# Performance work log

Hardware: AMD Instinct MI355X
Metric: run time of the kernel (lower is better)

## Reference

```python
import jax, jax.numpy as jnp
import numpy as np


def _conv(x, w, b, padding='SAME' if False else 'VALID'):
    # NCHW conv, OIHW weights
    out = jax.lax.conv_general_dilated(
        x, w, window_strides=(1, 1), padding=padding,
        dimension_numbers=('NCHW', 'OIHW', 'NCHW'))
    return out + b[None, :, None, None]


def setup_inputs() -> dict:
    key = jax.random.key(0)
    ks = jax.random.split(key, 14)
    s = lambda k, shape, scale=0.1: jax.random.normal(k, shape, dtype=jnp.float32) * scale
    return {
        'x': jax.random.normal(ks[0], (8, 16, 512, 512), dtype=jnp.float32),
        'y': jax.random.normal(ks[1], (8, 5, 512, 512), dtype=jnp.float32),
        'fuse_w': s(ks[2], (16, 5, 1, 1)),
        'fuse_b': s(ks[3], (16,)),
        'se_w1': s(ks[4], (16, 16)),
        'se_w2': s(ks[5], (5, 16)),
        'bd_w': s(ks[6], (2, 5, 1, 1)),
        'bd_b': s(ks[7], (2,)),
        'fc_w': s(ks[8], (16, 32, 3, 3)),
        'fc_b': s(ks[9], (16,)),
        'fm_w': s(ks[10], (2, 16, 1, 1)),
        'fm_b': s(ks[11], (2,)),
        'cv_w': s(ks[12], (16, 1, 1, 1)),
        'cv_b': s(ks[13], (16,)),
    }


def reference(x, y, fuse_w, fuse_b, se_w1, se_w2, bd_w, bd_b,
              fc_w, fc_b, fm_w, fm_b, cv_w, cv_b):
    # fuse: 1x1 conv 5->16 + ReLU
    fuse_box = jax.nn.relu(_conv(y, fuse_w, fuse_b, 'VALID'))  # [B,16,H,W]
    # global average pool -> SE mimic MLP -> sigmoid gate over 5 channels
    gap = jnp.mean(fuse_box, axis=(2, 3))                       # [B,16]
    se = jax.nn.sigmoid(jax.nn.relu(gap @ se_w1.T) @ se_w2.T)   # [B,5]
    feat_se = y * se[:, :, None, None]                          # [B,5,H,W]
    # boundary head: 1x1 conv 5->2, softmax over channel, take fg prob
    boundary = _conv(feat_se, bd_w, bd_b, 'VALID')              # [B,2,H,W]
    boundary_scale = jax.nn.softmax(boundary, axis=1)[:, 1:2]   # [B,1,H,W]
    # mask head: concat(x, fuse_box) -> 3x3 conv 32->16 + ReLU -> 1x1 conv 16->2
    feat_concat = jnp.concatenate([x, fuse_box], axis=1)        # [B,32,H,W]
    fcc = jax.nn.relu(_conv(feat_concat, fc_w, fc_b, 'SAME'))   # [B,16,H,W]
    mask = _conv(fcc, fm_w, fm_b, 'VALID')                      # [B,2,H,W]
    mask_scale = jax.nn.softmax(mask, axis=1)[:, 1:2]           # [B,1,H,W]
    # fused scale factor, clamp, expand to 16 channels via 1x1 conv
    scalefactor = jnp.clip(mask_scale + boundary_scale, 0.0, 1.0)
    return _conv(scalefactor, cv_w, cv_b, 'VALID')              # [B,16,H,W]
```

## Files before the change

### kernel.cpp

```cpp
#include <hip/hip_runtime.h>
#include <hip/hip_bf16.h>

#define HW 262144
#define IW 512
#define TW 64
#define TH 8
#define HLW 66
#define NHALO 660
#define ROWU 40

typedef __attribute__((ext_vector_type(8))) short short8;
typedef __attribute__((ext_vector_type(4))) float f32x4;
typedef __attribute__((ext_vector_type(4))) unsigned int uint4v;

static __device__ inline unsigned int bpack2(float a, float b) {
  __hip_bfloat16 ha = __float2bfloat16(a);
  __hip_bfloat16 hb = __float2bfloat16(b);
  unsigned short ua = *reinterpret_cast<unsigned short*>(&ha);
  unsigned short ub = *reinterpret_cast<unsigned short*>(&hb);
  return (unsigned int)ua | ((unsigned int)ub << 16);
}

__global__ __launch_bounds__(256) void k_gap(
    const float* __restrict__ y, const float* __restrict__ fuse_w,
    const float* __restrict__ fuse_b, float* __restrict__ partial) {
  __shared__ float fw[80], fb[16];
  __shared__ float red[4][16];
  int tid = threadIdx.x;
  if (tid < 80) fw[tid] = fuse_w[tid];
  if (tid < 16) fb[tid] = fuse_b[tid];
  __syncthreads();

  int b = blockIdx.x >> 7;
  int chunk = blockIdx.x & 127;
  const float* yb = y + (size_t)b * 5 * HW + chunk * 2048;

  float sums[16];
#pragma unroll
  for (int o = 0; o < 16; ++o) sums[o] = 0.f;

  for (int i = 0; i < 2048; i += 256) {
    int p = i + tid;
    float yv[5];
#pragma unroll
    for (int c = 0; c < 5; ++c) yv[c] = yb[c * HW + p];
#pragma unroll
    for (int o = 0; o < 16; ++o) {
      float a = fb[o];
#pragma unroll
      for (int c = 0; c < 5; ++c) a = fmaf(fw[o * 5 + c], yv[c], a);
      sums[o] += fmaxf(a, 0.f);
    }
  }

  int lane = tid & 63, wv = tid >> 6;
#pragma unroll
  for (int o = 0; o < 16; ++o) {
    float v = sums[o];
    for (int off = 32; off > 0; off >>= 1) v += __shfl_down(v, off);
    if (lane == 0) red[wv][o] = v;
  }
  __syncthreads();
  if (tid < 16)
    partial[blockIdx.x * 16 + tid] =
        red[0][tid] + red[1][tid] + red[2][tid] + red[3][tid];
}

__global__ __launch_bounds__(256) void k_se(
    const float* __restrict__ partial, const float* __restrict__ se_w1,
    const float* __restrict__ se_w2, const float* __restrict__ bd_w,
    float* __restrict__ bd_eff) {
  int tid = threadIdx.x;
  int b = tid >> 5, sub = tid & 31;
  float g[16];
#pragma unroll
  for (int c = 0; c < 16; ++c) g[c] = 0.f;
#pragma unroll
  for (int k = 0; k < 4; ++k) {
    const float* p = partial + (b * 128 + sub + k * 32) * 16;
#pragma unroll
    for (int c = 0; c < 16; ++c) g[c] += p[c];
  }
#pragma unroll
  for (int c = 0; c < 16; ++c) {
    float v = g[c];
    v += __shfl_xor(v, 1);  v += __shfl_xor(v, 2);
    v += __shfl_xor(v, 4);  v += __shfl_xor(v, 8);
    v += __shfl_xor(v, 16);
    g[c] = v * (1.f / 262144.f);
  }
  if (sub == 0) {
    float h[16];
#pragma unroll
    for (int j = 0; j < 16; ++j) {
      float s = 0.f;
#pragma unroll
      for (int c = 0; c < 16; ++c) s += g[c] * se_w1[j * 16 + c];
      h[j] = fmaxf(s, 0.f);
    }
#pragma unroll
    for (int i = 0; i < 5; ++i) {
      float s = 0.f;
#pragma unroll
      for (int j = 0; j < 16; ++j) s += h[j] * se_w2[i * 16 + j];
      float se = 1.f / (1.f + expf(-s));
      bd_eff[b * 10 + i]     = bd_w[i] * se;
      bd_eff[b * 10 + 5 + i] = bd_w[5 + i] * se;
    }
  }
}

__global__ void k_prep(const float* __restrict__ fc_w,
                       unsigned short* __restrict__ wTab) {
  int i = blockIdx.x * 256 + threadIdx.x;
  if (i < 4608) {
    int ci = i & 31, rest = i >> 5;
    int oc = rest & 15, s = rest >> 4;
    float v = fc_w[(oc * 32 + ci) * 9 + s];
    __hip_bfloat16 h = __float2bfloat16(v);
    wTab[i] = *reinterpret_cast<unsigned short*>(&h);
  }
}

__global__ __launch_bounds__(256) void k_pre(
    const float* __restrict__ y, const float* __restrict__ fuse_w,
    const float* __restrict__ fuse_b, const float* __restrict__ bd_eff,
    const float* __restrict__ bd_b, unsigned short* __restrict__ fuseP,
    float* __restrict__ bscaleP) {
  __shared__ float fw[80], fb[16], bde[10], bdb[2];
  int tid = threadIdx.x;
  int b = blockIdx.x >> 7;
  if (tid < 80) fw[tid] = fuse_w[tid];
  else if (tid < 96)  fb[tid - 80]  = fuse_b[tid - 80];
  else if (tid < 106) bde[tid - 96] = bd_eff[b * 10 + tid - 96];
  else if (tid < 108) bdb[tid - 106] = bd_b[tid - 106];
  __syncthreads();

  const float* yb = y + (size_t)b * 5 * HW;
  int gof0 = (blockIdx.x & 127) * 2048;
#pragma unroll 1
  for (int i = 0; i < 2048; i += 256) {
    int gofs = gof0 + i + tid;
    float yv[5];
#pragma unroll
    for (int c = 0; c < 5; ++c) yv[c] = yb[c * HW + gofs];
    float fo[16];
#pragma unroll
    for (int o = 0; o < 16; ++o) {
      float a = fb[o];
#pragma unroll
      for (int c = 0; c < 5; ++c) a = fmaf(fw[o * 5 + c], yv[c], a);
      fo[o] = fmaxf(a, 0.f);
    }
    size_t po = ((size_t)b * HW + gofs) * 16;
    uint4v v0 = {bpack2(fo[0], fo[1]), bpack2(fo[2], fo[3]),
                 bpack2(fo[4], fo[5]), bpack2(fo[6], fo[7])};
    uint4v v1 = {bpack2(fo[8], fo[9]), bpack2(fo[10], fo[11]),
                 bpack2(fo[12], fo[13]), bpack2(fo[14], fo[15])};
    *reinterpret_cast<uint4v*>(fuseP + po) = v0;
    *reinterpret_cast<uint4v*>(fuseP + po + 8) = v1;
    float bl0 = bdb[0], bl1 = bdb[1];
#pragma unroll
    for (int c = 0; c < 5; ++c) {
      bl0 = fmaf(bde[c], yv[c], bl0);
      bl1 = fmaf(bde[5 + c], yv[c], bl1);
    }
    bscaleP[(size_t)b * HW + gofs] = 1.f / (1.f + __expf(bl0 - bl1));
  }
}

template <int PRE>
__global__ __launch_bounds__(256) void k_main(
    const float* __restrict__ x, const float* __restrict__ y,
    const float* __restrict__ fuse_w, const float* __restrict__ fuse_b,
    const unsigned short* __restrict__ wTab,
    const unsigned short* __restrict__ fuseP,
    const float* __restrict__ bscaleP,
    const float* __restrict__ bd_eff, const float* __restrict__ bd_b,
    const float* __restrict__ fc_b,
    const float* __restrict__ fm_w, const float* __restrict__ fm_b,
    const float* __restrict__ cv_w, const float* __restrict__ cv_b,
    float* __restrict__ out) {
  __shared__ unsigned short tile[NHALO * ROWU];
  __shared__ float s_fw[80], s_fb[16], s_bde[10], s_bdb[2], s_fm[32],
      s_fmb[2], s_cv[16], s_cvb[16], s_fcb[16];

  int tid = threadIdx.x;
  int bsel = blockIdx.z;
  int h0 = blockIdx.y * TH;
  int w0 = blockIdx.x * TW;

  if (tid < 80) s_fw[tid] = fuse_w[tid];
  else if (tid < 96)  s_fb[tid - 80]   = fuse_b[tid - 80];
  else if (tid < 106) s_bde[tid - 96]  = bd_eff[bsel * 10 + tid - 96];
  else if (tid < 108) s_bdb[tid - 106] = bd_b[tid - 106];
  else if (tid < 140) s_fm[tid - 108]  = fm_w[tid - 108];
  else if (tid < 142) s_fmb[tid - 140] = fm_b[tid - 140];
  else if (tid < 158) s_cv[tid - 142]  = cv_w[tid - 142];
  else if (tid < 174) s_cvb[tid - 158] = cv_b[tid - 158];
  else if (tid < 190) s_fcb[tid - 174] = fc_b[tid - 174];

  int lane = tid & 63, wv = tid >> 6;
  int l15 = lane & 15, q = lane >> 4;

  short8 afrag[9];
#pragma unroll
  for (int s = 0; s < 9; ++s)
    afrag[s] = *reinterpret_cast<const short8*>(wTab + (s * 16 + l15) * 32 + q * 8);

  __syncthreads();

  const float* yb = y + (size_t)bsel * 5 * HW;
  const float* xb = x + (size_t)bsel * 16 * HW;
#pragma unroll 1
  for (int p = tid; p < NHALO; p += 256) {
    int hr = p / HLW, wc = p - hr * HLW;
    int gh = h0 - 1 + hr, gw = w0 - 1 + wc;
    bool valid = (gh >= 0) & (gh < IW) & (gw >= 0) & (gw < IW);
    uint4v* dst = reinterpret_cast<uint4v*>(&tile[p * ROWU]);
    if (valid) {
      int gofs = gh * IW + gw;
      if (PRE) {
        size_t po = ((size_t)bsel * HW + gofs) * 16;
        uint4v f0 = *reinterpret_cast<const uint4v*>(fuseP + po);
        uint4v f1 = *reinterpret_cast<const uint4v*>(fuseP + po + 8);
        float bsc = bscaleP[(size_t)bsel * HW + gofs];
        float a0 = xb[gofs],          a1 = xb[HW + gofs];
        float a2 = xb[2 * HW + gofs], a3 = xb[3 * HW + gofs];
        float a4 = xb[4 * HW + gofs], a5 = xb[5 * HW + gofs];
        float a6 = xb[6 * HW + gofs], a7 = xb[7 * HW + gofs];
        float a8 = xb[8 * HW + gofs],  a9 = xb[9 * HW + gofs];
        float aA = xb[10 * HW + gofs], aB = xb[11 * HW + gofs];
        float aC = xb[12 * HW + gofs], aD = xb[13 * HW + gofs];
        float aE = xb[14 * HW + gofs], aF = xb[15 * HW + gofs];
        dst[0] = uint4v{bpack2(a0, a1), bpack2(a2, a3),
                        bpack2(a4, a5), bpack2(a6, a7)};
        dst[1] = uint4v{bpack2(a8, a9), bpack2(aA, aB),
                        bpack2(aC, aD), bpack2(aE, aF)};
        dst[2] = f0;
        dst[3] = f1;
        *reinterpret_cast<float*>(&tile[p * ROWU + 32]) = bsc;
      } else {
        {
          float a0 = xb[gofs],          a1 = xb[HW + gofs];
          float a2 = xb[2 * HW + gofs], a3 = xb[3 * HW + gofs];
          float a4 = xb[4 * HW + gofs], a5 = xb[5 * HW + gofs];
          float a6 = xb[6 * HW + gofs], a7 = xb[7 * HW + gofs];
          dst[0] = uint4v{bpack2(a0, a1), bpack2(a2, a3),
                          bpack2(a4, a5), bpack2(a6, a7)};
        }
        {
          float a0 = xb[8 * HW + gofs],  a1 = xb[9 * HW + gofs];
          float a2 = xb[10 * HW + gofs], a3 = xb[11 * HW + gofs];
          float a4 = xb[12 * HW + gofs], a5 = xb[13 * HW + gofs];
          float a6 = xb[14 * HW + gofs], a7 = xb[15 * HW + gofs];
          dst[1] = uint4v{bpack2(a0, a1), bpack2(a2, a3),
                          bpack2(a4, a5), bpack2(a6, a7)};
        }
        float yv[5];
#pragma unroll
        for (int c = 0; c < 5; ++c) yv[c] = yb[c * HW + gofs];
        float fo[8];
#pragma unroll
        for (int o = 0; o < 8; ++o) {
          float a = s_fb[o];
#pragma unroll
          for (int c = 0; c < 5; ++c) a = fmaf(s_fw[o * 5 + c], yv[c], a);
          fo[o] = fmaxf(a, 0.f);
        }
        dst[2] = uint4v{bpack2(fo[0], fo[1]), bpack2(fo[2], fo[3]),
                        bpack2(fo[4], fo[5]), bpack2(fo[6], fo[7])};
#pragma unroll
        for (int o = 0; o < 8; ++o) {
          float a = s_fb[8 + o];
#pragma unroll
          for (int c = 0; c < 5; ++c) a = fmaf(s_fw[(8 + o) * 5 + c], yv[c], a);
          fo[o] = fmaxf(a, 0.f);
        }
        dst[3] = uint4v{bpack2(fo[0], fo[1]), bpack2(fo[2], fo[3]),
                        bpack2(fo[4], fo[5]), bpack2(fo[6], fo[7])};
        float bl0 = s_bdb[0], bl1 = s_bdb[1];
#pragma unroll
        for (int c = 0; c < 5; ++c) {
          bl0 = fmaf(s_bde[c], yv[c], bl0);
          bl1 = fmaf(s_bde[5 + c], yv[c], bl1);
        }
        *reinterpret_cast<float*>(&tile[p * ROWU + 32]) =
            1.f / (1.f + __expf(bl0 - bl1));
      }
    } else {
      uint4v z = {0, 0, 0, 0};
      dst[0] = z; dst[1] = z; dst[2] = z; dst[3] = z;
      *reinterpret_cast<float*>(&tile[p * ROWU + 32]) = 0.f;
    }
  }
  __syncthreads();

  const char* tb = reinterpret_cast<const char*>(tile);
  unsigned bofs[8];
  f32x4 acc[8];
#pragma unroll
  for (int g = 0; g < 8; ++g) {
    int row = 2 * wv + (g >> 2), c0 = (g & 3) * 16;
    bofs[g] = (unsigned)((row * HLW + c0 + l15) * (ROWU * 2) + q * 16);
    acc[g] = f32x4{0.f, 0.f, 0.f, 0.f};
  }
#pragma unroll
  for (int kh = 0; kh < 3; ++kh) {
#pragma unroll
    for (int kw = 0; kw < 3; ++kw) {
      short8 a = afrag[kh * 3 + kw];
#pragma unroll
      for (int g = 0; g < 8; ++g) {
        short8 bfr = *reinterpret_cast<const short8*>(
            tb + bofs[g] + (kh * HLW + kw) * (ROWU * 2));
        acc[g] = __builtin_amdgcn_mfma_f32_16x16x32_bf16(a, bfr, acc[g], 0, 0, 0);
      }
    }
  }

  float pm0[8], pm1[8];
#pragma unroll
  for (int g = 0; g < 8; ++g) {
    float p0 = 0.f, p1 = 0.f;
#pragma unroll
    for (int j = 0; j < 4; ++j) {
      int oc = q * 4 + j;
      float fv = fmaxf(acc[g][j] + s_fcb[oc], 0.f);
      p0 = fmaf(s_fm[oc], fv, p0);
      p1 = fmaf(s_fm[16 + oc], fv, p1);
    }
    pm0[g] = p0; pm1[g] = p1;
  }
#pragma unroll
  for (int g = 0; g < 8; ++g) pm0[g] += __shfl_xor(pm0[g], 16);
#pragma unroll
  for (int g = 0; g < 8; ++g) pm1[g] += __shfl_xor(pm1[g], 16);
#pragma unroll
  for (int g = 0; g < 8; ++g) pm0[g] += __shfl_xor(pm0[g], 32);
#pragma unroll
  for (int g = 0; g < 8; ++g) pm1[g] += __shfl_xor(pm1[g], 32);

  float sc[8];
#pragma unroll
  for (int g = 0; g < 8; ++g) {
    int row = 2 * wv + (g >> 2), c0 = (g & 3) * 16;
    float mscale =
        1.f / (1.f + __expf((pm0[g] + s_fmb[0]) - (pm1[g] + s_fmb[1])));
    float bsc = *reinterpret_cast<const float*>(
        tb + ((row + 1) * HLW + c0 + l15 + 1) * (ROWU * 2) + 64);
    sc[g] = fminf(fmaxf(mscale + bsc, 0.f), 1.f);
  }

  float* outb = out + (size_t)bsel * 16 * HW;
#pragma unroll
  for (int g = 0; g < 8; ++g) {
    int row = 2 * wv + (g >> 2), c0 = (g & 3) * 16;
    int gofs = (h0 + row) * IW + w0 + c0 + l15;
#pragma unroll
    for (int j = 0; j < 4; ++j) {
      int oc = q * 4 + j;
      outb[(size_t)oc * HW + gofs] = fmaf(s_cv[oc], sc[g], s_cvb[oc]);
    }
  }
}

extern "C" void kernel_launch(void* const* d_in, const int* in_sizes, int n_in,
                              void* d_out, int out_size, void* d_ws, size_t ws_size,
                              hipStream_t stream) {
  const float* x      = (const float*)d_in[0];
  const float* y      = (const float*)d_in[1];
  const float* fuse_w = (const float*)d_in[2];
  const float* fuse_b = (const float*)d_in[3];
  const float* se_w1  = (const float*)d_in[4];
  const float* se_w2  = (const float*)d_in[5];
  const float* bd_w   = (const float*)d_in[6];
  const float* bd_b   = (const float*)d_in[7];
  const float* fc_w   = (const float*)d_in[8];
  const float* fc_b   = (const float*)d_in[9];
  const float* fm_w   = (const float*)d_in[10];
  const float* fm_b   = (const float*)d_in[11];
  const float* cv_w   = (const float*)d_in[12];
  const float* cv_b   = (const float*)d_in[13];
  float* out = (float*)d_out;

  char* ws = (char*)d_ws;
  float* partial = (float*)ws;
  float* bd_eff  = partial + 1024 * 16;
  unsigned short* wTab = (unsigned short*)(ws + (1024 * 16 + 80) * 4);
  size_t fuse_off = (((1024 * 16 + 80) * 4 + 4608 * 2) + 255) & ~(size_t)255;
  unsigned short* fuseP = (unsigned short*)(ws + fuse_off);
  float* bscaleP = (float*)(ws + fuse_off + (size_t)2097152 * 32);
  size_t need = fuse_off + (size_t)2097152 * 32 + (size_t)2097152 * 4;
  bool pre = ws_size >= need;

  k_gap<<<1024, 256, 0, stream>>>(y, fuse_w, fuse_b, partial);
  k_se<<<1, 256, 0, stream>>>(partial, se_w1, se_w2, bd_w, bd_eff);
  k_prep<<<18, 256, 0, stream>>>(fc_w, wTab);
  if (pre) {
    k_pre<<<1024, 256, 0, stream>>>(y, fuse_w, fuse_b, bd_eff, bd_b, fuseP,
                                    bscaleP);
    k_main<1><<<dim3(8, 64, 8), 256, 0, stream>>>(
        x, y, fuse_w, fuse_b, wTab, fuseP, bscaleP, bd_eff, bd_b, fc_b, fm_w,
        fm_b, cv_w, cv_b, out);
  } else {
    k_main<0><<<dim3(8, 64, 8), 256, 0, stream>>>(
        x, y, fuse_w, fuse_b, wTab, fuseP, bscaleP, bd_eff, bd_b, fc_b, fm_w,
        fm_b, cv_w, cv_b, out);
  }
}
```

Measured before the change: 144.8 us.

## Pre-pack x and fuse outputs into zero-padded bf16 planes, drop LDS staging

Adds kernels that convert x into two zero-padded bf16 channel-8 planes and write the fuse activations into two more padded planes during the GAP pass. The main conv kernel then reads MFMA B fragments straight from global memory with no shared-memory halo tile or boundary checks. The boundary scale moves into its own kernel. The goal is to remove LDS staging, halo recomputation and the separate fuse recomputation pass. The cost is extra global traffic for the padded planes, several more launches, and reliance on cache hits for the 3x3 overlapping reads.

```diff
diff --git a/kernel.cpp b/kernel.cpp
--- a/kernel.cpp
+++ b/kernel.cpp
@@ -5,9 +5,8 @@
 #define IW 512
 #define TW 64
 #define TH 8
-#define HLW 66
-#define NHALO 660
-#define ROWU 40
+#define PW 514
+#define PP 264196
 
 typedef __attribute__((ext_vector_type(8))) short short8;
 typedef __attribute__((ext_vector_type(4))) float f32x4;
@@ -21,9 +20,48 @@
   return (unsigned int)ua | ((unsigned int)ub << 16);
 }
 
-__global__ __launch_bounds__(256) void k_gap(
+__global__ __launch_bounds__(256) void k_zero(uint4v* __restrict__ xP0,
+                                              uint4v* __restrict__ xP1,
+                                              uint4v* __restrict__ fP0,
+                                              uint4v* __restrict__ fP1) {
+  int pl = blockIdx.x >> 3, b = blockIdx.x & 7;
+  uint4v* base = (pl == 0 ? xP0 : pl == 1 ? xP1 : pl == 2 ? fP0 : fP1) +
+                 (size_t)b * PP;
+  uint4v z = {0, 0, 0, 0};
+  for (int i = threadIdx.x; i < 2052; i += 256) {
+    int pp;
+    if (i < 514) pp = i;
+    else if (i < 1028) pp = 513 * PW + (i - 514);
+    else if (i < 1540) pp = (i - 1028 + 1) * PW;
+    else pp = (i - 1540 + 1) * PW + 513;
+    base[pp] = z;
+  }
+}
+
+__global__ __launch_bounds__(256) void k_xc(const float* __restrict__ x,
+                                            uint4v* __restrict__ xP0,
+                                            uint4v* __restrict__ xP1) {
+  for (int it = 0; it < 4; ++it) {
+    int idx = blockIdx.x * 1024 + it * 256 + threadIdx.x;
+    int b = idx >> 18, gofs = idx & (HW - 1);
+    const float* xb = x + (size_t)b * 16 * HW + gofs;
+    int gh = gofs >> 9, gw = gofs & 511;
+    size_t pp = (size_t)b * PP + (gh + 1) * PW + gw + 1;
+    float a0 = xb[0],       a1 = xb[HW],      a2 = xb[2 * HW],  a3 = xb[3 * HW];
+    float a4 = xb[4 * HW],  a5 = xb[5 * HW],  a6 = xb[6 * HW],  a7 = xb[7 * HW];
+    xP0[pp] = uint4v{bpack2(a0, a1), bpack2(a2, a3), bpack2(a4, a5),
+                     bpack2(a6, a7)};
+    float b0 = xb[8 * HW],  b1 = xb[9 * HW],  b2 = xb[10 * HW], b3 = xb[11 * HW];
+    float b4 = xb[12 * HW], b5 = xb[13 * HW], b6 = xb[14 * HW], b7 = xb[15 * HW];
+    xP1[pp] = uint4v{bpack2(b0, b1), bpack2(b2, b3), bpack2(b4, b5),
+                     bpack2(b6, b7)};
+  }
+}
+
+__global__ __launch_bounds__(256) void k_fuse(
     const float* __restrict__ y, const float* __restrict__ fuse_w,
-    const float* __restrict__ fuse_b, float* __restrict__ partial) {
+    const float* __restrict__ fuse_b, uint4v* __restrict__ fP0,
+    uint4v* __restrict__ fP1, float* __restrict__ partial) {
   __shared__ float fw[80], fb[16];
   __shared__ float red[4][16];
   int tid = threadIdx.x;
@@ -31,26 +69,37 @@
   if (tid < 16) fb[tid] = fuse_b[tid];
   __syncthreads();
 
-  int b = blockIdx.x >> 7;
-  int chunk = blockIdx.x & 127;
-  const float* yb = y + (size_t)b * 5 * HW + chunk * 2048;
+  int b = blockIdx.x >> 7, chunk = blockIdx.x & 127;
+  const float* yb = y + (size_t)b * 5 * HW;
+  uint4v* f0 = fP0 + (size_t)b * PP;
+  uint4v* f1 = fP1 + (size_t)b * PP;
+  int gof0 = chunk * 2048;
 
   float sums[16];
 #pragma unroll
   for (int o = 0; o < 16; ++o) sums[o] = 0.f;
 
+#pragma unroll 1
   for (int i = 0; i < 2048; i += 256) {
-    int p = i + tid;
+    int gofs = gof0 + i + tid;
     float yv[5];
 #pragma unroll
-    for (int c = 0; c < 5; ++c) yv[c] = yb[c * HW + p];
+    for (int c = 0; c < 5; ++c) yv[c] = yb[c * HW + gofs];
+    float fo[16];
 #pragma unroll
     for (int o = 0; o < 16; ++o) {
       float a = fb[o];
 #pragma unroll
       for (int c = 0; c < 5; ++c) a = fmaf(fw[o * 5 + c], yv[c], a);
-      sums[o] += fmaxf(a, 0.f);
-    }
+      fo[o] = fmaxf(a, 0.f);
+      sums[o] += fo[o];
+    }
+    int gh = gofs >> 9, gw = gofs & 511;
+    int pp = (gh + 1) * PW + gw + 1;
+    f0[pp] = uint4v{bpack2(fo[0], fo[1]), bpack2(fo[2], fo[3]),
+                    bpack2(fo[4], fo[5]), bpack2(fo[6], fo[7])};
+    f1[pp] = uint4v{bpack2(fo[8], fo[9]), bpack2(fo[10], fo[11]),
+                    bpack2(fo[12], fo[13]), bpack2(fo[14], fo[15])};
   }
 
   int lane = tid & 63, wv = tid >> 6;
@@ -107,6 +156,32 @@
       bd_eff[b * 10 + i]     = bd_w[i] * se;
       bd_eff[b * 10 + 5 + i] = bd_w[5 + i] * se;
     }
+  }
+}
+
+__global__ __launch_bounds__(256) void k_bsc(const float* __restrict__ y,
+                                             const float* __restrict__ bd_eff,
+                                             const float* __restrict__ bd_b,
+                                             float* __restrict__ bscaleP) {
+  __shared__ float bde[10], bdb[2];
+  int tid = threadIdx.x;
+  int b = blockIdx.x >> 7, chunk = blockIdx.x & 127;
+  if (tid < 10) bde[tid] = bd_eff[b * 10 + tid];
+  if (tid < 2) bdb[tid] = bd_b[tid];
+  __syncthreads();
+  const float* yb = y + (size_t)b * 5 * HW;
+  int gof0 = chunk * 2048;
+#pragma unroll 1
+  for (int i = 0; i < 2048; i += 256) {
+    int gofs = gof0 + i + tid;
+    float bl0 = bdb[0], bl1 = bdb[1];
+#pragma unroll
+    for (int c = 0; c < 5; ++c) {
+      float yv = yb[c * HW + gofs];
+      bl0 = fmaf(bde[c], yv, bl0);
+      bl1 = fmaf(bde[5 + c], yv, bl1);
+    }
+    bscaleP[(size_t)b * HW + gofs] = 1.f / (1.f + __expf(bl0 - bl1));
   }
 }
 
@@ -122,60 +197,146 @@
   }
 }
 
-__global__ __launch_bounds__(256) void k_pre(
+__global__ __launch_bounds__(256) void k_main2(
+    const unsigned short* __restrict__ xP0, const unsigned short* __restrict__ xP1,
+    const unsigned short* __restrict__ fP0, const unsigned short* __restrict__ fP1,
+    const unsigned short* __restrict__ wTab, const float* __restrict__ bscaleP,
+    const float* __restrict__ fc_b, const float* __restrict__ fm_w,
+    const float* __restrict__ fm_b, const float* __restrict__ cv_w,
+    const float* __restrict__ cv_b, float* __restrict__ out) {
+  __shared__ float s_fm[32], s_fmb[2], s_cv[16], s_cvb[16], s_fcb[16];
+  int tid = threadIdx.x;
+  if (tid < 32) s_fm[tid] = fm_w[tid];
+  else if (tid < 34) s_fmb[tid - 32] = fm_b[tid - 32];
+  else if (tid < 50) s_cv[tid - 34]  = cv_w[tid - 34];
+  else if (tid < 66) s_cvb[tid - 50] = cv_b[tid - 50];
+  else if (tid < 82) s_fcb[tid - 66] = fc_b[tid - 66];
+
+  int bsel = blockIdx.z;
+  int h0 = blockIdx.y * TH;
+  int w0 = blockIdx.x * TW;
+  int lane = tid & 63, wv = tid >> 6;
+  int l15 = lane & 15, q = lane >> 4;
+
+  short8 afrag[9];
+#pragma unroll
+  for (int s = 0; s < 9; ++s)
+    afrag[s] = *reinterpret_cast<const short8*>(wTab + (s * 16 + l15) * 32 + q * 8);
+
+  const unsigned short* plane = q == 0 ? xP0 : q == 1 ? xP1 : q == 2 ? fP0 : fP1;
+  const short8* pl = reinterpret_cast<const short8*>(plane) + (size_t)bsel * PP;
+
+  __syncthreads();
+
+  int pb[8];
+  f32x4 acc[8];
+#pragma unroll
+  for (int g = 0; g < 8; ++g) {
+    int row = 2 * wv + (g >> 2), c0 = (g & 3) * 16;
+    pb[g] = (h0 + row) * PW + w0 + c0 + l15;
+    acc[g] = f32x4{0.f, 0.f, 0.f, 0.f};
+  }
+#pragma unroll
+  for (int kh = 0; kh < 3; ++kh) {
+#pragma unroll
+    for (int kw = 0; kw < 3; ++kw) {
+      short8 a = afrag[kh * 3 + kw];
+      short8 bf[8];
+#pragma unroll
+      for (int g = 0; g < 8; ++g) bf[g] = pl[pb[g] + kh * PW + kw];
+#pragma unroll
+      for (int g = 0; g < 8; ++g)
+        acc[g] = __builtin_amdgcn_mfma_f32_16x16x32_bf16(a, bf[g], acc[g], 0, 0, 0);
+    }
+  }
+
+  float pm0[8], pm1[8];
+#pragma unroll
+  for (int g = 0; g < 8; ++g) {
+    float p0 = 0.f, p1 = 0.f;
+#pragma unroll
+    for (int j = 0; j < 4; ++j) {
+      int oc = q * 4 + j;
+      float fv = fmaxf(acc[g][j] + s_fcb[oc], 0.f);
+      p0 = fmaf(s_fm[oc], fv, p0);
+      p1 = fmaf(s_fm[16 + oc], fv, p1);
+    }
+    pm0[g] = p0; pm1[g] = p1;
+  }
+#pragma unroll
+  for (int g = 0; g < 8; ++g) pm0[g] += __shfl_xor(pm0[g], 16);
+#pragma unroll
+  for (int g = 0; g < 8; ++g) pm1[g] += __shfl_xor(pm1[g], 16);
+#pragma unroll
+  for (int g = 0; g < 8; ++g) pm0[g] += __shfl_xor(pm0[g], 32);
+#pragma unroll
+  for (int g = 0; g < 8; ++g) pm1[g] += __shfl_xor(pm1[g], 32);
+
+  const float* bsb = bscaleP + (size_t)bsel * HW;
+  float* outb = out + (size_t)bsel * 16 * HW;
+#pragma unroll
+  for (int g = 0; g < 8; ++g) {
+    int row = 2 * wv + (g >> 2), c0 = (g & 3) * 16;
+    int gofs = (h0 + row) * IW + w0 + c0 + l15;
+    float mscale =
+        1.f / (1.f + __expf((pm0[g] + s_fmb[0]) - (pm1[g] + s_fmb[1])));
+    float sc = fminf(fmaxf(mscale + bsb[gofs], 0.f), 1.f);
+#pragma unroll
+    for (int j = 0; j < 4; ++j) {
+      int oc = q * 4 + j;
+      outb[(size_t)oc * HW + gofs] = fmaf(s_cv[oc], sc, s_cvb[oc]);
+    }
+  }
+}
+
+#define HLW 66
+#define NHALO 660
+#define ROWU 40
+
+__global__ __launch_bounds__(256) void k_gap(
     const float* __restrict__ y, const float* __restrict__ fuse_w,
-    const float* __restrict__ fuse_b, const float* __restrict__ bd_eff,
-    const float* __restrict__ bd_b, unsigned short* __restrict__ fuseP,
-    float* __restrict__ bscaleP) {
-  __shared__ float fw[80], fb[16], bde[10], bdb[2];
+    const float* __restrict__ fuse_b, float* __restrict__ partial) {
+  __shared__ float fw[80], fb[16];
+  __shared__ float red[4][16];
   int tid = threadIdx.x;
-  int b = blockIdx.x >> 7;
   if (tid < 80) fw[tid] = fuse_w[tid];
-  else if (tid < 96)  fb[tid - 80]  = fuse_b[tid - 80];
-  else if (tid < 106) bde[tid - 96] = bd_eff[b * 10 + tid - 96];
-  else if (tid < 108) bdb[tid - 106] = bd_b[tid - 106];
-  __syncthreads();
-
-  const float* yb = y + (size_t)b * 5 * HW;
-  int gof0 = (blockIdx.x & 127) * 2048;
-#pragma unroll 1
+  if (tid < 16) fb[tid] = fuse_b[tid];
+  __syncthreads();
+  int b = blockIdx.x >> 7, chunk = blockIdx.x & 127;
+  const float* yb = y + (size_t)b * 5 * HW + chunk * 2048;
+  float sums[16];
+#pragma unroll
+  for (int o = 0; o < 16; ++o) sums[o] = 0.f;
   for (int i = 0; i < 2048; i += 256) {
-    int gofs = gof0 + i + tid;
+    int p = i + tid;
     float yv[5];
 #pragma unroll
-    for (int c = 0; c < 5; ++c) yv[c] = yb[c * HW + gofs];
-    float fo[16];
+    for (int c = 0; c < 5; ++c) yv[c] = yb[c * HW + p];
 #pragma unroll
     for (int o = 0; o < 16; ++o) {
       float a = fb[o];
 #pragma unroll
       for (int c = 0; c < 5; ++c) a = fmaf(fw[o * 5 + c], yv[c], a);
-      fo[o] = fmaxf(a, 0.f);
-    }
-    size_t po = ((size_t)b * HW + gofs) * 16;
-    uint4v v0 = {bpack2(fo[0], fo[1]), bpack2(fo[2], fo[3]),
-                 bpack2(fo[4], fo[5]), bpack2(fo[6], fo[7])};
-    uint4v v1 = {bpack2(fo[8], fo[9]), bpack2(fo[10], fo[11]),
-                 bpack2(fo[12], fo[13]), bpack2(fo[14], fo[15])};
-    *reinterpret_cast<uint4v*>(fuseP + po) = v0;
-    *reinterpret_cast<uint4v*>(fuseP + po + 8) = v1;
-    float bl0 = bdb[0], bl1 = bdb[1];
-#pragma unroll
-    for (int c = 0; c < 5; ++c) {
-      bl0 = fmaf(bde[c], yv[c], bl0);
-      bl1 = fmaf(bde[5 + c], yv[c], bl1);
-    }
-    bscaleP[(size_t)b * HW + gofs] = 1.f / (1.f + __expf(bl0 - bl1));
-  }
-}
-
-template <int PRE>
-__global__ __launch_bounds__(256) void k_main(
+      sums[o] += fmaxf(a, 0.f);
+    }
+  }
+  int lane = tid & 63, wv = tid >> 6;
+#pragma unroll
+  for (int o = 0; o < 16; ++o) {
+    float v = sums[o];
+    for (int off = 32; off > 0; off >>= 1) v += __shfl_down(v, off);
+    if (lane == 0) red[wv][o] = v;
+  }
+  __syncthreads();
+  if (tid < 16)
+    partial[blockIdx.x * 16 + tid] =
+        red[0][tid] + red[1][tid] + red[2][tid] + red[3][tid];
+}
+
+__global__ __launch_bounds__(256) void k_main_fb(
     const float* __restrict__ x, const float* __restrict__ y,
     const float* __restrict__ fuse_w, const float* __restrict__ fuse_b,
     const unsigned short* __restrict__ wTab,
-    const unsigned short* __restrict__ fuseP,
-    const float* __restrict__ bscaleP,
     const float* __restrict__ bd_eff, const float* __restrict__ bd_b,
     const float* __restrict__ fc_b,
     const float* __restrict__ fm_w, const float* __restrict__ fm_b,
@@ -184,12 +345,8 @@
   __shared__ unsigned short tile[NHALO * ROWU];
   __shared__ float s_fw[80], s_fb[16], s_bde[10], s_bdb[2], s_fm[32],
       s_fmb[2], s_cv[16], s_cvb[16], s_fcb[16];
-
   int tid = threadIdx.x;
-  int bsel = blockIdx.z;
-  int h0 = blockIdx.y * TH;
-  int w0 = blockIdx.x * TW;
-
+  int bsel = blockIdx.z, h0 = blockIdx.y * TH, w0 = blockIdx.x * TW;
   if (tid < 80) s_fw[tid] = fuse_w[tid];
   else if (tid < 96)  s_fb[tid - 80]   = fuse_b[tid - 80];
   else if (tid < 106) s_bde[tid - 96]  = bd_eff[bsel * 10 + tid - 96];
@@ -199,17 +356,12 @@
   else if (tid < 158) s_cv[tid - 142]  = cv_w[tid - 142];
   else if (tid < 174) s_cvb[tid - 158] = cv_b[tid - 158];
   else if (tid < 190) s_fcb[tid - 174] = fc_b[tid - 174];
-
-  int lane = tid & 63, wv = tid >> 6;
-  int l15 = lane & 15, q = lane >> 4;
-
+  int lane = tid & 63, wv = tid >> 6, l15 = lane & 15, q = lane >> 4;
   short8 afrag[9];
 #pragma unroll
   for (int s = 0; s < 9; ++s)
     afrag[s] = *reinterpret_cast<const short8*>(wTab + (s * 16 + l15) * 32 + q * 8);
-
-  __syncthreads();
-
+  __syncthreads();
   const float* yb = y + (size_t)bsel * 5 * HW;
   const float* xb = x + (size_t)bsel * 16 * HW;
 #pragma unroll 1
@@ -220,74 +372,52 @@
     uint4v* dst = reinterpret_cast<uint4v*>(&tile[p * ROWU]);
     if (valid) {
       int gofs = gh * IW + gw;
-      if (PRE) {
-        size_t po = ((size_t)bsel * HW + gofs) * 16;
-        uint4v f0 = *reinterpret_cast<const uint4v*>(fuseP + po);
-        uint4v f1 = *reinterpret_cast<const uint4v*>(fuseP + po + 8);
-        float bsc = bscaleP[(size_t)bsel * HW + gofs];
+      {
         float a0 = xb[gofs],          a1 = xb[HW + gofs];
         float a2 = xb[2 * HW + gofs], a3 = xb[3 * HW + gofs];
         float a4 = xb[4 * HW + gofs], a5 = xb[5 * HW + gofs];
         float a6 = xb[6 * HW + gofs], a7 = xb[7 * HW + gofs];
-        float a8 = xb[8 * HW + gofs],  a9 = xb[9 * HW + gofs];
-        float aA = xb[10 * HW + gofs], aB = xb[11 * HW + gofs];
-        float aC = xb[12 * HW + gofs], aD = xb[13 * HW + gofs];
-        float aE = xb[14 * HW + gofs], aF = xb[15 * HW + gofs];
         dst[0] = uint4v{bpack2(a0, a1), bpack2(a2, a3),
                         bpack2(a4, a5), bpack2(a6, a7)};
-        dst[1] = uint4v{bpack2(a8, a9), bpack2(aA, aB),
-                        bpack2(aC, aD), bpack2(aE, aF)};
-        dst[2] = f0;
-        dst[3] = f1;
-        *reinterpret_cast<float*>(&tile[p * ROWU + 32]) = bsc;
-      } else {
-        {
-          float a0 = xb[gofs],          a1 = xb[HW + gofs];
-          float a2 = xb[2 * HW + gofs], a3 = xb[3 * HW + gofs];
-          float a4 = xb[4 * HW + gofs], a5 = xb[5 * HW + gofs];
-          float a6 = xb[6 * HW + gofs], a7 = xb[7 * HW + gofs];
-          dst[0] = uint4v{bpack2(a0, a1), bpack2(a2, a3),
-                          bpack2(a4, a5), bpack2(a6, a7)};
-        }
-        {
-          float a0 = xb[8 * HW + gofs],  a1 = xb[9 * HW + gofs];
-          float a2 = xb[10 * HW + gofs], a3 = xb[11 * HW + gofs];
-          float a4 = xb[12 * HW + gofs], a5 = xb[13 * HW + gofs];
-          float a6 = xb[14 * HW + gofs], a7 = xb[15 * HW + gofs];
-          dst[1] = uint4v{bpack2(a0, a1), bpack2(a2, a3),
-                          bpack2(a4, a5), bpack2(a6, a7)};
-        }
-        float yv[5];
-#pragma unroll
-        for (int c = 0; c < 5; ++c) yv[c] = yb[c * HW + gofs];
-        float fo[8];
-#pragma unroll
-        for (int o = 0; o < 8; ++o) {
-          float a = s_fb[o];
-#pragma unroll
-          for (int c = 0; c < 5; ++c) a = fmaf(s_fw[o * 5 + c], yv[c], a);
-          fo[o] = fmaxf(a, 0.f);
-        }
-        dst[2] = uint4v{bpack2(fo[0], fo[1]), bpack2(fo[2], fo[3]),
-                        bpack2(fo[4], fo[5]), bpack2(fo[6], fo[7])};
-#pragma unroll
-        for (int o = 0; o < 8; ++o) {
-          float a = s_fb[8 + o];
-#pragma unroll
-          for (int c = 0; c < 5; ++c) a = fmaf(s_fw[(8 + o) * 5 + c], yv[c], a);
-          fo[o] = fmaxf(a, 0.f);
-        }
-        dst[3] = uint4v{bpack2(fo[0], fo[1]), bpack2(fo[2], fo[3]),
-                        bpack2(fo[4], fo[5]), bpack2(fo[6], fo[7])};
-        float bl0 = s_bdb[0], bl1 = s_bdb[1];
-#pragma unroll
-        for (int c = 0; c < 5; ++c) {
-          bl0 = fmaf(s_bde[c], yv[c], bl0);
-          bl1 = fmaf(s_bde[5 + c], yv[c], bl1);
-        }
-        *reinterpret_cast<float*>(&tile[p * ROWU + 32]) =
-            1.f / (1.f + __expf(bl0 - bl1));
       }
+      {
+        float a0 = xb[8 * HW + gofs],  a1 = xb[9 * HW + gofs];
+        float a2 = xb[10 * HW + gofs], a3 = xb[11 * HW + gofs];
+        float a4 = xb[12 * HW + gofs], a5 = xb[13 * HW + gofs];
+        float a6 = xb[14 * HW + gofs], a7 = xb[15 * HW + gofs];
+        dst[1] = uint4v{bpack2(a0, a1), bpack2(a2, a3),
+                        bpack2(a4, a5), bpack2(a6, a7)};
+      }
+      float yv[5];
+#pragma unroll
+      for (int c = 0; c < 5; ++c) yv[c] = yb[c * HW + gofs];
+      float fo[8];
+#pragma unroll
+      for (int o = 0; o < 8; ++o) {
+        float a = s_fb[o];
+#pragma unroll
+        for (int c = 0; c < 5; ++c) a = fmaf(s_fw[o * 5 + c], yv[c], a);
+        fo[o] = fmaxf(a, 0.f);
+      }
+      dst[2] = uint4v{bpack2(fo[0], fo[1]), bpack2(fo[2], fo[3]),
+                      bpack2(fo[4], fo[5]), bpack2(fo[6], fo[7])};
+#pragma unroll
+      for (int o = 0; o < 8; ++o) {
+        float a = s_fb[8 + o];
+#pragma unroll
+        for (int c = 0; c < 5; ++c) a = fmaf(s_fw[(8 + o) * 5 + c], yv[c], a);
+        fo[o] = fmaxf(a, 0.f);
+      }
+      dst[3] = uint4v{bpack2(fo[0], fo[1]), bpack2(fo[2], fo[3]),
+                      bpack2(fo[4], fo[5]), bpack2(fo[6], fo[7])};
+      float bl0 = s_bdb[0], bl1 = s_bdb[1];
+#pragma unroll
+      for (int c = 0; c < 5; ++c) {
+        bl0 = fmaf(s_bde[c], yv[c], bl0);
+        bl1 = fmaf(s_bde[5 + c], yv[c], bl1);
+      }
+      *reinterpret_cast<float*>(&tile[p * ROWU + 32]) =
+          1.f / (1.f + __expf(bl0 - bl1));
     } else {
       uint4v z = {0, 0, 0, 0};
       dst[0] = z; dst[1] = z; dst[2] = z; dst[3] = z;
@@ -295,7 +425,6 @@
     }
   }
   __syncthreads();
-
   const char* tb = reinterpret_cast<const char*>(tile);
   unsigned bofs[8];
   f32x4 acc[8];
@@ -318,7 +447,6 @@
       }
     }
   }
-
   float pm0[8], pm1[8];
 #pragma unroll
   for (int g = 0; g < 8; ++g) {
@@ -340,27 +468,20 @@
   for (int g = 0; g < 8; ++g) pm0[g] += __shfl_xor(pm0[g], 32);
 #pragma unroll
   for (int g = 0; g < 8; ++g) pm1[g] += __shfl_xor(pm1[g], 32);
-
-  float sc[8];
+  float* outb = out + (size_t)bsel * 16 * HW;
 #pragma unroll
   for (int g = 0; g < 8; ++g) {
     int row = 2 * wv + (g >> 2), c0 = (g & 3) * 16;
+    int gofs = (h0 + row) * IW + w0 + c0 + l15;
     float mscale =
         1.f / (1.f + __expf((pm0[g] + s_fmb[0]) - (pm1[g] + s_fmb[1])));
     float bsc = *reinterpret_cast<const float*>(
         tb + ((row + 1) * HLW + c0 + l15 + 1) * (ROWU * 2) + 64);
-    sc[g] = fminf(fmaxf(mscale + bsc, 0.f), 1.f);
-  }
-
-  float* outb = out + (size_t)bsel * 16 * HW;
-#pragma unroll
-  for (int g = 0; g < 8; ++g) {
-    int row = 2 * wv + (g >> 2), c0 = (g & 3) * 16;
-    int gofs = (h0 + row) * IW + w0 + c0 + l15;
+    float sc = fminf(fmaxf(mscale + bsc, 0.f), 1.f);
 #pragma unroll
     for (int j = 0; j < 4; ++j) {
       int oc = q * 4 + j;
-      outb[(size_t)oc * HW + gofs] = fmaf(s_cv[oc], sc[g], s_cvb[oc]);
+      outb[(size_t)oc * HW + gofs] = fmaf(s_cv[oc], sc, s_cvb[oc]);
     }
   }
 }
@@ -387,25 +508,33 @@
   char* ws = (char*)d_ws;
   float* partial = (float*)ws;
   float* bd_eff  = partial + 1024 * 16;
-  unsigned short* wTab = (unsigned short*)(ws + (1024 * 16 + 80) * 4);
-  size_t fuse_off = (((1024 * 16 + 80) * 4 + 4608 * 2) + 255) & ~(size_t)255;
-  unsigned short* fuseP = (unsigned short*)(ws + fuse_off);
-  float* bscaleP = (float*)(ws + fuse_off + (size_t)2097152 * 32);
-  size_t need = fuse_off + (size_t)2097152 * 32 + (size_t)2097152 * 4;
-  bool pre = ws_size >= need;
-
-  k_gap<<<1024, 256, 0, stream>>>(y, fuse_w, fuse_b, partial);
-  k_se<<<1, 256, 0, stream>>>(partial, se_w1, se_w2, bd_w, bd_eff);
-  k_prep<<<18, 256, 0, stream>>>(fc_w, wTab);
-  if (pre) {
-    k_pre<<<1024, 256, 0, stream>>>(y, fuse_w, fuse_b, bd_eff, bd_b, fuseP,
-                                    bscaleP);
-    k_main<1><<<dim3(8, 64, 8), 256, 0, stream>>>(
-        x, y, fuse_w, fuse_b, wTab, fuseP, bscaleP, bd_eff, bd_b, fc_b, fm_w,
-        fm_b, cv_w, cv_b, out);
+  unsigned short* wTab = (unsigned short*)(ws + 65856);
+  size_t off = 75264;
+  const size_t PLB = (size_t)8 * PP * 16;
+  unsigned short* xP0 = (unsigned short*)(ws + off);
+  unsigned short* xP1 = (unsigned short*)(ws + off + PLB);
+  unsigned short* fP0 = (unsigned short*)(ws + off + 2 * PLB);
+  unsigned short* fP1 = (unsigned short*)(ws + off + 3 * PLB);
+  float* bscaleP = (float*)(ws + off + 4 * PLB);
+  size_t need = off + 4 * PLB + (size_t)8 * HW * 4;
+
+  if (ws_size >= need) {
+    k_zero<<<32, 256, 0, stream>>>((uint4v*)xP0, (uint4v*)xP1, (uint4v*)fP0,
+                                   (uint4v*)fP1);
+    k_xc<<<2048, 256, 0, stream>>>(x, (uint4v*)xP0, (uint4v*)xP1);
+    k_fuse<<<1024, 256, 0, stream>>>(y, fuse_w, fuse_b, (uint4v*)fP0,
+                                     (uint4v*)fP1, partial);
+    k_se<<<1, 256, 0, stream>>>(partial, se_w1, se_w2, bd_w, bd_eff);
+    k_bsc<<<1024, 256, 0, stream>>>(y, bd_eff, bd_b, bscaleP);
+    k_prep<<<18, 256, 0, stream>>>(fc_w, wTab);
+    k_main2<<<dim3(8, 64, 8), 256, 0, stream>>>(
+        xP0, xP1, fP0, fP1, wTab, bscaleP, fc_b, fm_w, fm_b, cv_w, cv_b, out);
   } else {
-    k_main<0><<<dim3(8, 64, 8), 256, 0, stream>>>(
-        x, y, fuse_w, fuse_b, wTab, fuseP, bscaleP, bd_eff, bd_b, fc_b, fm_w,
-        fm_b, cv_w, cv_b, out);
-  }
-}
+    k_gap<<<1024, 256, 0, stream>>>(y, fuse_w, fuse_b, partial);
+    k_se<<<1, 256, 0, stream>>>(partial, se_w1, se_w2, bd_w, bd_eff);
+    k_prep<<<18, 256, 0, stream>>>(fc_w, wTab);
+    k_main_fb<<<dim3(8, 64, 8), 256, 0, stream>>>(
+        x, y, fuse_w, fuse_b, wTab, bd_eff, bd_b, fc_b, fm_w, fm_b, cv_w, cv_b,
+        out);
+  }
+}
```

After: 202.4 us. 39.8% more time.
